# Performance work log

Hardware: AMD Instinct MI355X
Metric: run time of the kernel (lower is better)

The kernel has to match this reference:

```python
import jax, jax.numpy as jnp
import numpy as np

N_NODES = 50000
N_EDGES = 800000
IN_CH, HID, LAT = 256, 128, 64


def setup_inputs() -> dict:
    key = jax.random.key(0)
    k1, k2, k3, k4 = jax.random.split(key, 4)
    x = jax.random.normal(k1, (N_NODES, IN_CH), dtype=jnp.float32)
    edge_index = jax.random.randint(k2, (2, N_EDGES), 0, N_NODES, dtype=jnp.int64)
    W1 = jax.random.normal(k3, (IN_CH, HID), dtype=jnp.float32) * (1.0 / np.sqrt(IN_CH))
    b1 = jnp.zeros((HID,), dtype=jnp.float32)
    W2 = jax.random.normal(k4, (HID, LAT), dtype=jnp.float32) * (1.0 / np.sqrt(HID))
    b2 = jnp.zeros((LAT,), dtype=jnp.float32)
    return {"x": x, "edge_index": edge_index, "W1": W1, "b1": b1, "W2": W2, "b2": b2}


def gcn_conv(x, src, dst, deg_inv_sqrt, W, b):
    # PyG GCNConv: h = x @ W; out[dst] += d_dst^-1/2 * d_src^-1/2 * h[src]; + bias
    h = x @ W                                   # [N, out]
    norm = deg_inv_sqrt[src] * deg_inv_sqrt[dst]  # [E+N]
    msg = h[src] * norm[:, None]                # [E+N, out] (gather + scale)
    out = jax.ops.segment_sum(msg, dst, num_segments=x.shape[0])
    return out + b


def reference(x, edge_index, W1, b1, W2, b2):
    n = x.shape[0]
    loop = jnp.arange(n, dtype=edge_index.dtype)
    # add self loops (GCNConv default)
    src = jnp.concatenate([edge_index[0], loop])
    dst = jnp.concatenate([edge_index[1], loop])
    deg = jax.ops.segment_sum(jnp.ones_like(dst, dtype=x.dtype), dst, num_segments=n)
    deg_inv_sqrt = jnp.where(deg > 0, jax.lax.rsqrt(deg), 0.0)
    h = jax.nn.relu(gcn_conv(x, src, dst, deg_inv_sqrt, W1, b1))
    h = jax.nn.relu(gcn_conv(h, src, dst, deg_inv_sqrt, W2, b2))
    return h
```

## Files before the change

kernel.cpp:

```cpp
#include <hip/hip_runtime.h>

#define N_NODES 50000
#define N_EDGES 800000
#define IN_CH 256
#define HID 128
#define LAT 64
#define CAP 64
#define NBIN 196
#define BINCAP 4864

typedef __attribute__((ext_vector_type(8))) short short8;
typedef __attribute__((ext_vector_type(16))) float f32x16;

static __device__ __forceinline__ unsigned short bf16_rne(float x) {
    unsigned u = __float_as_uint(x);
    unsigned r = (u + 0x7FFFu + ((u >> 16) & 1u)) >> 16;
    return (unsigned short)r;
}
static __device__ __forceinline__ float bf16_to_f(unsigned short h) {
    return __uint_as_float(((unsigned)h) << 16);
}

static __device__ __forceinline__ void add8(uint4 p, float* a) {
    a[0] += __uint_as_float(p.x << 16);
    a[1] += __uint_as_float(p.x & 0xFFFF0000u);
    a[2] += __uint_as_float(p.y << 16);
    a[3] += __uint_as_float(p.y & 0xFFFF0000u);
    a[4] += __uint_as_float(p.z << 16);
    a[5] += __uint_as_float(p.z & 0xFFFF0000u);
    a[6] += __uint_as_float(p.w << 16);
    a[7] += __uint_as_float(p.w & 0xFFFF0000u);
}
static __device__ __forceinline__ void fma8(uint4 p, float m, float* a) {
    a[0] = fmaf(m, __uint_as_float(p.x << 16), a[0]);
    a[1] = fmaf(m, __uint_as_float(p.x & 0xFFFF0000u), a[1]);
    a[2] = fmaf(m, __uint_as_float(p.y << 16), a[2]);
    a[3] = fmaf(m, __uint_as_float(p.y & 0xFFFF0000u), a[3]);
    a[4] = fmaf(m, __uint_as_float(p.z << 16), a[4]);
    a[5] = fmaf(m, __uint_as_float(p.z & 0xFFFF0000u), a[5]);
    a[6] = fmaf(m, __uint_as_float(p.w << 16), a[6]);
    a[7] = fmaf(m, __uint_as_float(p.w & 0xFFFF0000u), a[7]);
}

template <int K, int NN>
static __device__ __forceinline__ void split_store(const float* __restrict__ W,
                                                   unsigned short* __restrict__ Wf, int i) {
    constexpr int CT = NN / 32;
    int k = i / NN, n = i % NN;
    float w = W[i];
    unsigned short hi = bf16_rne(w);
    unsigned short lo = bf16_rne(w - bf16_to_f(hi));
    size_t off = ((size_t)((k >> 4) * CT + (n >> 5)) * 64 + ((n & 31) + 32 * ((k >> 3) & 1))) * 8 + (k & 7);
    Wf[off] = hi;
    Wf[(size_t)K * NN + off] = lo;
}

__global__ __launch_bounds__(256) void prep_kernel(const float* __restrict__ W1,
                                                   const float* __restrict__ W2,
                                                   int* __restrict__ binCnt,
                                                   unsigned short* __restrict__ W1f,
                                                   unsigned short* __restrict__ W2f) {
    int i = blockIdx.x * blockDim.x + threadIdx.x;
    if (i < NBIN) binCnt[i] = 0;
    if (i < IN_CH * HID) split_store<IN_CH, HID>(W1, W1f, i);
    if (i < HID * LAT) split_store<HID, LAT>(W2, W2f, i);
}

__global__ __launch_bounds__(256) void fill1_kernel(const int* __restrict__ ei,
                                                    int* __restrict__ binCnt,
                                                    unsigned int* __restrict__ binBuf, int E) {
    __shared__ int hist[NBIN];
    __shared__ int base[NBIN];
    const int tid = threadIdx.x;
    for (int i = tid; i < NBIN; i += 256) hist[i] = 0;
    __syncthreads();

    const int e0 = blockIdx.x * 2048 + tid;
    unsigned int pk[8];
    int bn[8], ofs[8];
#pragma unroll
    for (int i = 0; i < 8; ++i) {
        int e = e0 + 256 * i;
        bool v = e < E;
        int s = v ? ei[e] : 0;
        int d = v ? ei[E + e] : 0;
        bn[i] = d >> 8;
        pk[i] = (unsigned int)s | ((unsigned int)(d & 255) << 16);
        ofs[i] = v ? atomicAdd(&hist[bn[i]], 1) : -1;
    }
    __syncthreads();
    for (int i = tid; i < NBIN; i += 256)
        base[i] = hist[i] ? atomicAdd(&binCnt[i], hist[i]) : 0;
    __syncthreads();
#pragma unroll
    for (int i = 0; i < 8; ++i) {
        if (ofs[i] >= 0) {
            int p = base[bn[i]] + ofs[i];
            if (p < BINCAP) binBuf[(size_t)bn[i] * BINCAP + p] = pk[i];
        }
    }
}

__global__ __launch_bounds__(256) void fill2_kernel(const int* __restrict__ binCnt,
                                                    const unsigned int* __restrict__ binBuf,
                                                    int* __restrict__ cnt,
                                                    unsigned short* __restrict__ colb) {
    __shared__ int lcnt[256];
    const int b = blockIdx.x;
    const int tid = threadIdx.x;
    lcnt[tid] = 0;
    __syncthreads();
    int n = binCnt[b]; if (n > BINCAP) n = BINCAP;
    const int node0 = b << 8;
    const unsigned int* bb = binBuf + (size_t)b * BINCAP;
    int n4 = n & ~3;
    for (int i = tid * 4; i < n4; i += 1024) {
        uint4 pk4 = *(const uint4*)(bb + i);
        unsigned int pks[4] = {pk4.x, pk4.y, pk4.z, pk4.w};
#pragma unroll
        for (int q = 0; q < 4; ++q) {
            unsigned int pk = pks[q];
            int local = pk >> 16;
            int s = pk & 0xFFFF;
            int slot = atomicAdd(&lcnt[local], 1);
            if (slot < CAP) colb[(size_t)(node0 + local) * CAP + slot] = (unsigned short)s;
        }
    }
    for (int i = n4 + tid; i < n; i += 256) {
        unsigned int pk = bb[i];
        int local = pk >> 16;
        int s = pk & 0xFFFF;
        int slot = atomicAdd(&lcnt[local], 1);
        if (slot < CAP) colb[(size_t)(node0 + local) * CAP + slot] = (unsigned short)s;
    }
    __syncthreads();
    int node = node0 + tid;
    if (node < N_NODES) cnt[node] = lcnt[tid];
}

template <int K, int NN, bool AFP32>
__global__ __launch_bounds__(256) void gemm_kernel(const void* __restrict__ Av,
                                                   const unsigned short* __restrict__ Wf,
                                                   const int* __restrict__ cnt,
                                                   unsigned short* __restrict__ C, int M) {
    constexpr int CT = NN / 32;
    constexpr int NT = (NN == 128) ? 2 : 1;
    __shared__ unsigned short As[4 * 512];
    __shared__ unsigned short Bs[2 * 2 * CT * 512];

    const int tid = threadIdx.x;
    const int lane = tid & 63;
    const int w = tid >> 6;
    const int row0 = blockIdx.x * 64;
    const int rt = w >> 1;
    const int ct0 = (NN == 128) ? ((w & 1) * 2) : (w & 1);

    f32x16 acc[NT];
#pragma unroll
    for (int nt = 0; nt < NT; ++nt)
#pragma unroll
        for (int q = 0; q < 16; ++q) acc[nt][q] = 0.0f;

    for (int kt = 0; kt < K; kt += 32) {
        {
            int m = tid >> 2, kc = tid & 3;
            int row = row0 + m; if (row >= M) row = M - 1;
            int s = kc >> 1, half = kc & 1, t = m >> 5;
            int ln = (m & 31) + 32 * half;
            uint4 v;
            if constexpr (AFP32) {
                const float* A = (const float*)Av;
                const float4 v0 = *(const float4*)(A + (size_t)row * K + kt + kc * 8);
                const float4 v1 = *(const float4*)(A + (size_t)row * K + kt + kc * 8 + 4);
                v.x = (unsigned)bf16_rne(v0.x) | ((unsigned)bf16_rne(v0.y) << 16);
                v.y = (unsigned)bf16_rne(v0.z) | ((unsigned)bf16_rne(v0.w) << 16);
                v.z = (unsigned)bf16_rne(v1.x) | ((unsigned)bf16_rne(v1.y) << 16);
                v.w = (unsigned)bf16_rne(v1.z) | ((unsigned)bf16_rne(v1.w) << 16);
            } else {
                const unsigned short* A = (const unsigned short*)Av;
                v = *(const uint4*)(A + (size_t)row * K + kt + kc * 8);
            }
            *(uint4*)&As[((s * 2 + t) << 9) + (ln << 3)] = v;
        }
        {
            const int sg0 = kt >> 4;
#pragma unroll
            for (int i0 = 0; i0 < CT * 256; i0 += 256) {
                int i = i0 + tid;
                int psl = i / (CT * 64), rem = i % (CT * 64);
                int p = psl >> 1, sl = psl & 1;
                const uint4* src = (const uint4*)(Wf + (size_t)p * K * NN + (size_t)(sg0 + sl) * CT * 512);
                ((uint4*)Bs)[i] = src[rem];
            }
        }
        __syncthreads();

#pragma unroll
        for (int sl = 0; sl < 2; ++sl) {
            short8 a = *(const short8*)&As[((sl * 2 + rt) << 9) + (lane << 3)];
            short8 bh[NT], bl[NT];
#pragma unroll
            for (int nt = 0; nt < NT; ++nt) {
                bh[nt] = *(const short8*)&Bs[((sl * CT + ct0 + nt) << 9) + (lane << 3)];
                bl[nt] = *(const short8*)&Bs[(((2 + sl) * CT + ct0 + nt) << 9) + (lane << 3)];
            }
#pragma unroll
            for (int nt = 0; nt < NT; ++nt) {
                acc[nt] = __builtin_amdgcn_mfma_f32_32x32x16_bf16(a, bh[nt], acc[nt], 0, 0, 0);
                acc[nt] = __builtin_amdgcn_mfma_f32_32x32x16_bf16(a, bl[nt], acc[nt], 0, 0, 0);
            }
        }
        __syncthreads();
    }

#pragma unroll
    for (int r = 0; r < 16; ++r) {
        int rowl = rt * 32 + (r & 3) + 8 * (r >> 2) + 4 * (lane >> 5);
        int row = row0 + rowl;
        if (row < M) {
            float sc = rsqrtf((float)cnt[row] + 1.0f);
#pragma unroll
            for (int nt = 0; nt < NT; ++nt) {
                int col = (ct0 + nt) * 32 + (lane & 31);
                C[(size_t)row * NN + col] = bf16_rne(acc[nt][r] * sc);
            }
        }
    }
}

template <int C, bool OBF16>
__global__ __launch_bounds__(256) void agg_kernel(const int* __restrict__ cnt,
                                                  const unsigned short* __restrict__ colb,
                                                  const unsigned short* __restrict__ hs,
                                                  const float* __restrict__ bias,
                                                  void* __restrict__ outv, int N) {
    constexpr int LPN = C / 8;
    constexpr int NPB = 256 / LPN;
    const int node = blockIdx.x * NPB + (int)(threadIdx.x / LPN);
    const int u = threadIdx.x % LPN;
    if (node >= N) return;

    const unsigned short* __restrict__ hbase = hs + u * 8;

    uint4 selfp = *(const uint4*)(hbase + (size_t)node * C);
    int deg = cnt[node];
    const unsigned short* __restrict__ cb = colb + (size_t)node * CAP;
    int kk = deg < CAP ? deg : CAP;

    float acc[8];
#pragma unroll
    for (int q = 0; q < 8; ++q) acc[q] = 0.0f;
    add8(selfp, acc);

    int j = 0;
    for (; j + 4 <= kk; j += 4) {
        ushort4 s4 = *(const ushort4*)(cb + j);
        uint4 p0 = *(const uint4*)(hbase + (size_t)s4.x * C);
        uint4 p1 = *(const uint4*)(hbase + (size_t)s4.y * C);
        uint4 p2 = *(const uint4*)(hbase + (size_t)s4.z * C);
        uint4 p3 = *(const uint4*)(hbase + (size_t)s4.w * C);
        add8(p0, acc); add8(p1, acc); add8(p2, acc); add8(p3, acc);
    }
    if (j < kk) {
        ushort4 s4 = *(const ushort4*)(cb + j);
        bool v1 = (j + 1) < kk, v2 = (j + 2) < kk;
        int t0 = s4.x;
        int t1 = v1 ? (int)s4.y : 0;
        int t2 = v2 ? (int)s4.z : 0;
        uint4 p0 = *(const uint4*)(hbase + (size_t)t0 * C);
        uint4 p1 = *(const uint4*)(hbase + (size_t)t1 * C);
        uint4 p2 = *(const uint4*)(hbase + (size_t)t2 * C);
        add8(p0, acc);
        fma8(p1, v1 ? 1.0f : 0.0f, acc);
        fma8(p2, v2 ? 1.0f : 0.0f, acc);
    }

    float di = rsqrtf((float)deg + 1.0f);
    const float4 b0 = *(const float4*)(bias + u * 8);
    const float4 b1 = *(const float4*)(bias + u * 8 + 4);
    float o[8];
    o[0] = fmaxf(fmaf(di, acc[0], b0.x), 0.0f);
    o[1] = fmaxf(fmaf(di, acc[1], b0.y), 0.0f);
    o[2] = fmaxf(fmaf(di, acc[2], b0.z), 0.0f);
    o[3] = fmaxf(fmaf(di, acc[3], b0.w), 0.0f);
    o[4] = fmaxf(fmaf(di, acc[4], b1.x), 0.0f);
    o[5] = fmaxf(fmaf(di, acc[5], b1.y), 0.0f);
    o[6] = fmaxf(fmaf(di, acc[6], b1.z), 0.0f);
    o[7] = fmaxf(fmaf(di, acc[7], b1.w), 0.0f);

    if constexpr (OBF16) {
        uint4 st;
        st.x = (unsigned)bf16_rne(o[0]) | ((unsigned)bf16_rne(o[1]) << 16);
        st.y = (unsigned)bf16_rne(o[2]) | ((unsigned)bf16_rne(o[3]) << 16);
        st.z = (unsigned)bf16_rne(o[4]) | ((unsigned)bf16_rne(o[5]) << 16);
        st.w = (unsigned)bf16_rne(o[6]) | ((unsigned)bf16_rne(o[7]) << 16);
        *(uint4*)((unsigned short*)outv + (size_t)node * C + u * 8) = st;
    } else {
        float* op = (float*)outv + (size_t)node * C + u * 8;
        float4 o0 = {o[0], o[1], o[2], o[3]};
        float4 o1 = {o[4], o[5], o[6], o[7]};
        *(float4*)op = o0;
        *(float4*)(op + 4) = o1;
    }
}

extern "C" void kernel_launch(void* const* d_in, const int* in_sizes, int n_in,
                              void* d_out, int out_size, void* d_ws, size_t ws_size,
                              hipStream_t stream) {
    const float* x  = (const float*)d_in[0];
    const int*   ei = (const int*)d_in[1];
    const float* W1 = (const float*)d_in[2];
    const float* b1 = (const float*)d_in[3];
    const float* W2 = (const float*)d_in[4];
    const float* b2 = (const float*)d_in[5];

    const int N = N_NODES, E = N_EDGES;

    char* ws = (char*)d_ws;
    size_t off = 0;
    auto alloc = [&](size_t bytes) {
        void* p = ws + off;
        off = (off + bytes + 255) & ~(size_t)255;
        return p;
    };
    int*            cnt    = (int*)alloc((size_t)N * 4);
    unsigned short* colb   = (unsigned short*)alloc((size_t)N * CAP * 2);
    int*            binCnt = (int*)alloc((size_t)NBIN * 4);
    unsigned int*   binBuf = (unsigned int*)alloc((size_t)NBIN * BINCAP * 4);
    unsigned short* W1f    = (unsigned short*)alloc((size_t)2 * IN_CH * HID * 2);
    unsigned short* W2f    = (unsigned short*)alloc((size_t)2 * HID * LAT * 2);
    unsigned short* h1s    = (unsigned short*)alloc((size_t)N * HID * 2);
    unsigned short* act1   = (unsigned short*)alloc((size_t)N * HID * 2);
    unsigned short* h2s    = h1s;

    prep_kernel<<<(N + 255) / 256, 256, 0, stream>>>(W1, W2, binCnt, W1f, W2f);
    fill1_kernel<<<(E + 2047) / 2048, 256, 0, stream>>>(ei, binCnt, binBuf, E);
    fill2_kernel<<<NBIN, 256, 0, stream>>>(binCnt, binBuf, cnt, colb);

    gemm_kernel<IN_CH, HID, true><<<(N + 63) / 64, 256, 0, stream>>>(x, W1f, cnt, h1s, N);
    agg_kernel<HID, true><<<(N + 15) / 16, 256, 0, stream>>>(cnt, colb, h1s, b1, act1, N);

    gemm_kernel<HID, LAT, false><<<(N + 63) / 64, 256, 0, stream>>>(act1, W2f, cnt, h2s, N);
    agg_kernel<LAT, false><<<(N + 31) / 32, 256, 0, stream>>>(cnt, colb, h2s, b2, d_out, N);
}
```

Measured before the change: 190.5 us.

## Store features in 32-column chunked layout so aggregation gathers fit cache

```diff
diff --git a/kernel.cpp b/kernel.cpp
--- a/kernel.cpp
+++ b/kernel.cpp
@@ -178,7 +178,7 @@
                 v.w = (unsigned)bf16_rne(v1.z) | ((unsigned)bf16_rne(v1.w) << 16);
             } else {
                 const unsigned short* A = (const unsigned short*)Av;
-                v = *(const uint4*)(A + (size_t)row * K + kt + kc * 8);
+                v = *(const uint4*)(A + ((size_t)(kt >> 5) * M + row) * 32 + kc * 8);
             }
             *(uint4*)&As[((s * 2 + t) << 9) + (ln << 3)] = v;
         }
@@ -221,8 +221,8 @@
             float sc = rsqrtf((float)cnt[row] + 1.0f);
 #pragma unroll
             for (int nt = 0; nt < NT; ++nt) {
-                int col = (ct0 + nt) * 32 + (lane & 31);
-                C[(size_t)row * NN + col] = bf16_rne(acc[nt][r] * sc);
+                int p = ct0 + nt;
+                C[((size_t)p * M + row) * 32 + (lane & 31)] = bf16_rne(acc[nt][r] * sc);
             }
         }
     }
@@ -234,15 +234,15 @@
                                                   const unsigned short* __restrict__ hs,
                                                   const float* __restrict__ bias,
                                                   void* __restrict__ outv, int N) {
-    constexpr int LPN = C / 8;
-    constexpr int NPB = 256 / LPN;
-    const int node = blockIdx.x * NPB + (int)(threadIdx.x / LPN);
-    const int u = threadIdx.x % LPN;
+    const int NB = (N_NODES + 63) / 64;
+    const int chunk = blockIdx.x / NB;
+    const int node = (blockIdx.x % NB) * 64 + (int)(threadIdx.x >> 2);
+    const int u = threadIdx.x & 3;
     if (node >= N) return;
 
-    const unsigned short* __restrict__ hbase = hs + u * 8;
-
-    uint4 selfp = *(const uint4*)(hbase + (size_t)node * C);
+    const unsigned short* __restrict__ hbase = hs + (size_t)chunk * N * 32 + u * 8;
+
+    uint4 selfp = *(const uint4*)(hbase + (size_t)node * 32);
     int deg = cnt[node];
     const unsigned short* __restrict__ cb = colb + (size_t)node * CAP;
     int kk = deg < CAP ? deg : CAP;
@@ -255,10 +255,10 @@
     int j = 0;
     for (; j + 4 <= kk; j += 4) {
         ushort4 s4 = *(const ushort4*)(cb + j);
-        uint4 p0 = *(const uint4*)(hbase + (size_t)s4.x * C);
-        uint4 p1 = *(const uint4*)(hbase + (size_t)s4.y * C);
-        uint4 p2 = *(const uint4*)(hbase + (size_t)s4.z * C);
-        uint4 p3 = *(const uint4*)(hbase + (size_t)s4.w * C);
+        uint4 p0 = *(const uint4*)(hbase + (size_t)s4.x * 32);
+        uint4 p1 = *(const uint4*)(hbase + (size_t)s4.y * 32);
+        uint4 p2 = *(const uint4*)(hbase + (size_t)s4.z * 32);
+        uint4 p3 = *(const uint4*)(hbase + (size_t)s4.w * 32);
         add8(p0, acc); add8(p1, acc); add8(p2, acc); add8(p3, acc);
     }
     if (j < kk) {
@@ -267,17 +267,17 @@
         int t0 = s4.x;
         int t1 = v1 ? (int)s4.y : 0;
         int t2 = v2 ? (int)s4.z : 0;
-        uint4 p0 = *(const uint4*)(hbase + (size_t)t0 * C);
-        uint4 p1 = *(const uint4*)(hbase + (size_t)t1 * C);
-        uint4 p2 = *(const uint4*)(hbase + (size_t)t2 * C);
+        uint4 p0 = *(const uint4*)(hbase + (size_t)t0 * 32);
+        uint4 p1 = *(const uint4*)(hbase + (size_t)t1 * 32);
+        uint4 p2 = *(const uint4*)(hbase + (size_t)t2 * 32);
         add8(p0, acc);
         fma8(p1, v1 ? 1.0f : 0.0f, acc);
         fma8(p2, v2 ? 1.0f : 0.0f, acc);
     }
 
     float di = rsqrtf((float)deg + 1.0f);
-    const float4 b0 = *(const float4*)(bias + u * 8);
-    const float4 b1 = *(const float4*)(bias + u * 8 + 4);
+    const float4 b0 = *(const float4*)(bias + chunk * 32 + u * 8);
+    const float4 b1 = *(const float4*)(bias + chunk * 32 + u * 8 + 4);
     float o[8];
     o[0] = fmaxf(fmaf(di, acc[0], b0.x), 0.0f);
     o[1] = fmaxf(fmaf(di, acc[1], b0.y), 0.0f);
@@ -294,9 +294,9 @@
         st.y = (unsigned)bf16_rne(o[2]) | ((unsigned)bf16_rne(o[3]) << 16);
         st.z = (unsigned)bf16_rne(o[4]) | ((unsigned)bf16_rne(o[5]) << 16);
         st.w = (unsigned)bf16_rne(o[6]) | ((unsigned)bf16_rne(o[7]) << 16);
-        *(uint4*)((unsigned short*)outv + (size_t)node * C + u * 8) = st;
+        *(uint4*)((unsigned short*)outv + ((size_t)chunk * N + node) * 32 + u * 8) = st;
     } else {
-        float* op = (float*)outv + (size_t)node * C + u * 8;
+        float* op = (float*)outv + (size_t)node * C + chunk * 32 + u * 8;
         float4 o0 = {o[0], o[1], o[2], o[3]};
         float4 o1 = {o[4], o[5], o[6], o[7]};
         *(float4*)op = o0;
@@ -315,6 +315,7 @@
     const float* b2 = (const float*)d_in[5];
 
     const int N = N_NODES, E = N_EDGES;
+    const int NB = (N + 63) / 64;
 
     char* ws = (char*)d_ws;
     size_t off = 0;
@@ -338,8 +339,8 @@
     fill2_kernel<<<NBIN, 256, 0, stream>>>(binCnt, binBuf, cnt, colb);
 
     gemm_kernel<IN_CH, HID, true><<<(N + 63) / 64, 256, 0, stream>>>(x, W1f, cnt, h1s, N);
-    agg_kernel<HID, true><<<(N + 15) / 16, 256, 0, stream>>>(cnt, colb, h1s, b1, act1, N);
+    agg_kernel<HID, true><<<4 * NB, 256, 0, stream>>>(cnt, colb, h1s, b1, act1, N);
 
     gemm_kernel<HID, LAT, false><<<(N + 63) / 64, 256, 0, stream>>>(act1, W2f, cnt, h2s, N);
-    agg_kernel<LAT, false><<<(N + 31) / 32, 256, 0, stream>>>(cnt, colb, h2s, b2, d_out, N);
-}
+    agg_kernel<LAT, false><<<2 * NB, 256, 0, stream>>>(cnt, colb, h2s, b2, d_out, N);
+}
```

Result: slower. 213.8 us (+12.2%).
